# Optimization experiments

Hardware: AMD Instinct MI355X
Metric: run time of the kernel (lower is better)

## Reference

```python
import math
import jax, jax.numpy as jnp
import numpy as np

NHID = 1024
HEADS = 16
SEQ = 1024
BATCH = 8


def setup_inputs() -> dict:
    key = jax.random.key(0)
    ks = jax.random.split(key, 12)
    s = 0.02
    inp = {
        "query": jax.random.normal(ks[0], (SEQ, BATCH, NHID), jnp.float32),
        "key": jax.random.normal(ks[1], (SEQ, BATCH, NHID), jnp.float32),
        "value": jax.random.normal(ks[2], (SEQ, BATCH, NHID), jnp.float32),
        "qs_p": jax.random.normal(ks[3], (1, 1, NHID), jnp.float32) * s,
        "ks_p": jax.random.normal(ks[4], (1, 1, NHID), jnp.float32) * s,
        "vs_p": jax.random.normal(ks[5], (1, 1, NHID), jnp.float32) * s,
        "Wq": jax.random.normal(ks[6], (NHID, NHID), jnp.float32) * s,
        "bq": jax.random.normal(ks[7], (NHID,), jnp.float32) * s,
        "Wzf": jax.random.normal(ks[8], (2 * NHID, NHID), jnp.float32) * s,
        "bzf": jax.random.normal(ks[9], (2 * NHID,), jnp.float32) * s,
    }
    # additive causal mask, viewed as (1,1,S,S) and added to scores
    causal = jnp.triu(jnp.ones((SEQ, SEQ), jnp.float32), k=1) * (-1e9)
    inp["attn_mask"] = causal
    return inp


def reference(query, key, value, qs_p, ks_p, vs_p, Wq, bq, Wzf, bzf, attn_mask):
    nhid = NHID
    heads = HEADS
    dim = nhid // heads

    # sigmoid gates on Q/K/V scales
    qs = jax.nn.sigmoid(qs_p)              # (1,1,nhid)
    ks_g = jax.nn.sigmoid(ks_p)
    vs_in = jax.nn.sigmoid(vs_p)

    # QRNNLayer(window=1, output_gate=False) on single-step vs:
    # z = tanh(Wz vs + bz), f = sigmoid(Wf vs + bf), h = f * z (h0 = 0)
    zf = jnp.einsum('abn,mn->abm', vs_in, Wzf) + bzf   # (1,1,2*nhid)
    z = jnp.tanh(zf[..., :nhid])
    f = jax.nn.sigmoid(zf[..., nhid:])
    vs = f * z                                          # (1,1,nhid)

    # q projection (k,v have no Linear with defaults)
    q_lin = jnp.einsum('sbn,mn->sbm', query, Wq) + bq

    q = qs * q_lin       # (S,B,nhid)
    k = ks_g * key
    v = vs * value

    # seq-first -> batch-first, split heads
    def split_heads(t):
        t = t.transpose(1, 0, 2)                         # (B,S,nhid)
        B, S, _ = t.shape
        return t.reshape(B, S, heads, dim).transpose(0, 2, 1, 3)  # (B,H,S,d)

    qh, kh, vh = split_heads(q), split_heads(k), split_heads(v)

    scores = jnp.einsum('bhqd,bhkd->bhqk', qh, kh) / math.sqrt(dim)
    scores = scores + attn_mask[None, None]              # (B,H,S,S)
    weights = jax.nn.softmax(scores, axis=-1)
    mix = jnp.einsum('bhqk,bhkd->bhqd', weights, vh)     # (B,H,S,d)

    B = mix.shape[0]
    mix = mix.transpose(0, 2, 1, 3).reshape(B, -1, nhid)  # (B,S,nhid)
    mix = mix.transpose(1, 0, 2)                          # (S,B,nhid) seq-first
    return mix, weights
```

## Files before the change

kernel.cpp:

```cpp
#include <hip/hip_runtime.h>

typedef unsigned short u16;
typedef unsigned int   u32;
typedef float  f32x4  __attribute__((ext_vector_type(4)));
typedef short  bf16x8 __attribute__((ext_vector_type(8)));
typedef unsigned short u16x8 __attribute__((ext_vector_type(8)));
typedef unsigned short u16x4 __attribute__((ext_vector_type(4)));
typedef unsigned int   u32x2 __attribute__((ext_vector_type(2)));

#define DEV __device__ __forceinline__

constexpr int S  = 1024;
constexpr int BB = 8;
constexpr int NH = 1024;
constexpr int H  = 16;

DEV u16 f2bf(float f) {
  union { float f; unsigned u; } v{f};
  unsigned r = v.u + 0x7FFFu + ((v.u >> 16) & 1u);
  return (u16)(r >> 16);
}
DEV float sigm(float x) { return 1.0f / (1.0f + __expf(-x)); }

DEV void gload_lds16(const void* g, void* l) {
  __builtin_amdgcn_global_load_lds(
      (const __attribute__((address_space(1))) unsigned int*)g,
      (__attribute__((address_space(3))) unsigned int*)l, 16, 0, 0);
}

__global__ __launch_bounds__(256) void k_gates(
    const float* __restrict__ qs_p, const float* __restrict__ ks_p,
    const float* __restrict__ vs_p, const float* __restrict__ Wq,
    const float* __restrict__ bq,  const float* __restrict__ Wzf,
    const float* __restrict__ bzf,
    float* __restrict__ ksg, float* __restrict__ vsg,
    float* __restrict__ bq2, u16* __restrict__ wq_bf)
{
  int m = blockIdx.x * 4 + (threadIdx.x >> 6);
  int l = threadIdx.x & 63;
  const float* wz = Wzf + (size_t)m * NH;
  const float* wf = Wzf + (size_t)(m + NH) * NH;
  int base = l * 16;
  float za = 0.f, fa = 0.f;
#pragma unroll
  for (int i = 0; i < 16; i += 4) {
    float4 vp  = *(const float4*)(vs_p + base + i);
    float4 wzv = *(const float4*)(wz + base + i);
    float4 wfv = *(const float4*)(wf + base + i);
    float v0 = sigm(vp.x), v1 = sigm(vp.y), v2 = sigm(vp.z), v3 = sigm(vp.w);
    za += v0 * wzv.x + v1 * wzv.y + v2 * wzv.z + v3 * wzv.w;
    fa += v0 * wfv.x + v1 * wfv.y + v2 * wfv.z + v3 * wfv.w;
  }
#pragma unroll
  for (int off = 1; off < 64; off <<= 1) {
    za += __shfl_xor(za, off);
    fa += __shfl_xor(fa, off);
  }
  float z   = tanhf(za + bzf[m]);
  float f   = sigm(fa + bzf[m + NH]);
  float qsm = sigm(qs_p[m]);
  if (l == 0) {
    ksg[m] = sigm(ks_p[m]);
    vsg[m] = f * z;
    bq2[m] = qsm * bq[m];
  }
  const float* wqr = Wq + (size_t)m * NH;
  u16* dst = wq_bf + (size_t)m * NH + base;
#pragma unroll
  for (int i = 0; i < 16; i += 4) {
    float4 wv = *(const float4*)(wqr + base + i);
    u16x4 o;
    o[0] = f2bf(qsm * wv.x); o[1] = f2bf(qsm * wv.y);
    o[2] = f2bf(qsm * wv.z); o[3] = f2bf(qsm * wv.w);
    *(u16x4*)(dst + i) = o;
  }
}

__global__ __launch_bounds__(256) void k_prep(
    const float* __restrict__ query, const float* __restrict__ key,
    const float* __restrict__ value, const float* __restrict__ ksg,
    const float* __restrict__ vsg,
    u16* __restrict__ qx, u16* __restrict__ kout, u16* __restrict__ vout)
{
  __shared__ float tile[64][65];
  size_t idx = ((size_t)blockIdx.x * 256 + threadIdx.x) * 8;
  {
    float4 a = *(const float4*)(query + idx);
    float4 b = *(const float4*)(query + idx + 4);
    u16x8 o;
    o[0] = f2bf(a.x); o[1] = f2bf(a.y); o[2] = f2bf(a.z); o[3] = f2bf(a.w);
    o[4] = f2bf(b.x); o[5] = f2bf(b.y); o[6] = f2bf(b.z); o[7] = f2bf(b.w);
    *(u16x8*)(qx + idx) = o;
  }
  {
    int n0 = (int)(idx & 1023);
    int b  = (int)((idx >> 10) & 7);
    int s  = (int)(idx >> 13);
    float4 a  = *(const float4*)(key + idx);
    float4 c  = *(const float4*)(key + idx + 4);
    float4 g0 = *(const float4*)(ksg + n0);
    float4 g1 = *(const float4*)(ksg + n0 + 4);
    int h = n0 >> 6, d0 = n0 & 63;
    u16* dst = kout + (((size_t)(b * H + h) * S + s) * 64 + d0);
    u16x8 o;
    o[0] = f2bf(a.x * g0.x); o[1] = f2bf(a.y * g0.y);
    o[2] = f2bf(a.z * g0.z); o[3] = f2bf(a.w * g0.w);
    o[4] = f2bf(c.x * g1.x); o[5] = f2bf(c.y * g1.y);
    o[6] = f2bf(c.z * g1.z); o[7] = f2bf(c.w * g1.w);
    *(u16x8*)dst = o;
  }
  if (blockIdx.x < 2048) {
    int bh = blockIdx.x >> 4, kt = blockIdx.x & 15;
    int b = bh >> 4, h = bh & 15;
    int t = threadIdx.x;
    int sp = t >> 2, c0 = (t & 3) * 16;
    const float* src = value + ((size_t)(kt * 64 + sp) * (BB * NH) + b * NH + h * 64 + c0);
#pragma unroll
    for (int i = 0; i < 16; i += 4) {
      float4 v = *(const float4*)(src + i);
      float4 g = *(const float4*)(vsg + h * 64 + c0 + i);
      tile[sp][c0 + i + 0] = v.x * g.x;
      tile[sp][c0 + i + 1] = v.y * g.y;
      tile[sp][c0 + i + 2] = v.z * g.z;
      tile[sp][c0 + i + 3] = v.w * g.w;
    }
    __syncthreads();
    int d = t >> 2, s0 = (t & 3) * 16;
    u16* dst = vout + (((size_t)bh * 16 + kt) * 64 + d) * 64 + s0;
    u16x8 o0, o1;
#pragma unroll
    for (int i = 0; i < 8; ++i) o0[i] = f2bf(tile[s0 + i][d]);
#pragma unroll
    for (int i = 0; i < 8; ++i) o1[i] = f2bf(tile[s0 + 8 + i][d]);
    *(u16x8*)dst       = o0;
    *(u16x8*)(dst + 8) = o1;
  }
}

__global__ __launch_bounds__(256) void k_gemm_q(
    const u16* __restrict__ qx, const u16* __restrict__ wq,
    const float* __restrict__ bq2, u16* __restrict__ qws)
{
  __shared__ __align__(16) u16 As[128 * 64];
  __shared__ __align__(16) u16 Bs[128 * 64];
  int bid = blockIdx.x;
  int swz = (bid & 7) * 64 + (bid >> 3);
  int bx = swz & 7, by = swz >> 3;
  int tid = threadIdx.x, w = tid >> 6, l = tid & 63;
  int wr = w >> 1, wc = w & 1;
  f32x4 zero4 = {0.f, 0.f, 0.f, 0.f};
  f32x4 acc[4][4];
#pragma unroll
  for (int fi = 0; fi < 4; ++fi)
#pragma unroll
    for (int fj = 0; fj < 4; ++fj) acc[fi][fj] = zero4;

  for (int kt = 0; kt < 16; ++kt) {
    __syncthreads();
#pragma unroll
    for (int ii = 0; ii < 4; ++ii) {
      int i = w * 4 + ii;
      int row = i * 8 + (l >> 3);
      int blk = (l & 7) ^ (row & 7);
      gload_lds16(qx + ((size_t)(by * 128 + row) * 1024 + kt * 64 + blk * 8), &As[i * 512]);
      gload_lds16(wq + ((size_t)(bx * 128 + row) * 1024 + kt * 64 + blk * 8), &Bs[i * 512]);
    }
    __syncthreads();
#pragma unroll
    for (int kk = 0; kk < 2; ++kk) {
      bf16x8 av[4], bv[4];
#pragma unroll
      for (int f = 0; f < 4; ++f) {
        int ar = wr * 64 + f * 16 + (l & 15);
        av[f] = *(const bf16x8*)&As[ar * 64 + ((((kk << 2) + (l >> 4)) ^ (ar & 7)) << 3)];
        int br = wc * 64 + f * 16 + (l & 15);
        bv[f] = *(const bf16x8*)&Bs[br * 64 + ((((kk << 2) + (l >> 4)) ^ (br & 7)) << 3)];
      }
#pragma unroll
      for (int fi = 0; fi < 4; ++fi)
#pragma unroll
        for (int fj = 0; fj < 4; ++fj)
          acc[fi][fj] = __builtin_amdgcn_mfma_f32_16x16x32_bf16(av[fi], bv[fj], acc[fi][fj], 0, 0, 0);
    }
  }
#pragma unroll
  for (int fi = 0; fi < 4; ++fi) {
    int grb = by * 128 + wr * 64 + fi * 16 + ((l >> 4) << 2);
#pragma unroll
    for (int fj = 0; fj < 4; ++fj) {
      int mcol = bx * 128 + wc * 64 + fj * 16 + (l & 15);
      float badd = bq2[mcol];
      int h = mcol >> 6, d = mcol & 63;
#pragma unroll
      for (int r = 0; r < 4; ++r) {
        int gr = grb + r;
        int srow = gr >> 3, bb = gr & 7;
        qws[((size_t)(bb * H + h) * S + srow) * 64 + d] = f2bf(acc[fi][fj][r] + badd);
      }
    }
  }
}

__global__ __launch_bounds__(256) void k_attn(
    const u16* __restrict__ qws, const u16* __restrict__ kws,
    const u16* __restrict__ vtw, float* __restrict__ mix,
    float* __restrict__ wout)
{
  __shared__ __align__(16) u16 Ks[2][64 * 64];
  __shared__ __align__(16) u16 Vs[2][64 * 64];
  __shared__ __align__(16) u16 Ps[4][16 * 64];
  int bid = blockIdx.x;
  int swz = (bid & 7) * 256 + (bid >> 3);
  int qt = swz & 15, bh = swz >> 4;
  int tid = threadIdx.x, w = tid >> 6, l = tid & 63;
  int g = l >> 4, lq = l & 15;
  int q0 = qt * 64;
  int myq = q0 + 16 * w + lq;
  float* wbase = wout + (size_t)bh * S * S;

  auto stageK = [&](int kt, int buf) {
#pragma unroll
    for (int ii = 0; ii < 2; ++ii) {
      int i = w * 2 + ii;
      int row = i * 8 + (l >> 3);
      int blk = (l & 7) ^ (row & 7);
      gload_lds16(kws + ((size_t)bh * S + kt * 64 + row) * 64 + blk * 8, &Ks[buf][i * 512]);
    }
  };
  auto stageV = [&](int kt, int buf) {
#pragma unroll
    for (int ii = 0; ii < 2; ++ii) {
      int i = w * 2 + ii;
      int row = i * 8 + (l >> 3);
      int blk = (l & 7) ^ (row & 7);
      gload_lds16(vtw + (((size_t)bh * 16 + kt) * 64 + row) * 64 + blk * 8, &Vs[buf][i * 512]);
    }
  };

#pragma unroll
  for (int ii = 0; ii < 2; ++ii) {
    int i = w * 2 + ii;
    int row = i * 8 + (l >> 3);
    int blk = (l & 7) ^ (row & 7);
    gload_lds16(qws + ((size_t)bh * S + q0 + row) * 64 + blk * 8, &Ks[0][i * 512]);
  }
  asm volatile("s_waitcnt vmcnt(0)" ::: "memory");
  __builtin_amdgcn_sched_barrier(0);
  bf16x8 qa[2];
#pragma unroll
  for (int kk = 0; kk < 2; ++kk) {
    int qr = 16 * w + lq;
    qa[kk] = *(const bf16x8*)&Ks[0][qr * 64 + ((((kk << 2) + g) ^ (qr & 7)) << 3)];
  }
  asm volatile("s_waitcnt lgkmcnt(0)" ::: "memory");
  __builtin_amdgcn_sched_barrier(0);
  __builtin_amdgcn_s_barrier();

  stageK(0, 0);
  float lsum = 0.f;
  int cur = 0;
  for (int kt = 0; kt <= qt; ++kt) {
    asm volatile("s_waitcnt vmcnt(0)" ::: "memory");
    __builtin_amdgcn_sched_barrier(0);
    __builtin_amdgcn_s_barrier();
    __builtin_amdgcn_sched_barrier(0);
    if (kt < qt) stageK(kt + 1, cur ^ 1);
    __builtin_amdgcn_sched_barrier(0);
    f32x4 sacc[4];
    f32x4 zero4 = {0.f, 0.f, 0.f, 0.f};
#pragma unroll
    for (int fj = 0; fj < 4; ++fj) sacc[fj] = zero4;
#pragma unroll
    for (int kk = 0; kk < 2; ++kk)
#pragma unroll
      for (int fj = 0; fj < 4; ++fj) {
        int kr = fj * 16 + lq;
        bf16x8 kb = *(const bf16x8*)&Ks[cur][kr * 64 + ((((kk << 2) + g) ^ (kr & 7)) << 3)];
        sacc[fj] = __builtin_amdgcn_mfma_f32_16x16x32_bf16(kb, qa[kk], sacc[fj], 0, 0, 0);
      }
    if (kt < qt) {
#pragma unroll
      for (int fj = 0; fj < 4; ++fj)
#pragma unroll
        for (int r = 0; r < 4; ++r) lsum += __expf(sacc[fj][r] * 0.125f);
    } else {
#pragma unroll
      for (int fj = 0; fj < 4; ++fj)
#pragma unroll
        for (int r = 0; r < 4; ++r) {
          int ki = kt * 64 + fj * 16 + 4 * g + r;
          if (ki <= myq) lsum += __expf(sacc[fj][r] * 0.125f);
        }
    }
    cur ^= 1;
  }
  lsum += __shfl_xor(lsum, 16);
  lsum += __shfl_xor(lsum, 32);
  float invl = 1.0f / lsum;

  __builtin_amdgcn_s_barrier();

  stageK(0, 0);
  stageV(0, 0);
  cur = 0;
  f32x4 oacc[4];
  {
    f32x4 zero4 = {0.f, 0.f, 0.f, 0.f};
#pragma unroll
    for (int db = 0; db < 4; ++db) oacc[db] = zero4;
  }
  char* pb = (char*)&Ps[w][0];
  int pswz = (lq & 7) * 16;
  for (int kt = 0; kt <= qt; ++kt) {
    if (kt > 0) asm volatile("s_waitcnt vmcnt(4)" ::: "memory");
    else        asm volatile("s_waitcnt vmcnt(0)" ::: "memory");
    __builtin_amdgcn_sched_barrier(0);
    __builtin_amdgcn_s_barrier();
    __builtin_amdgcn_sched_barrier(0);
    if (kt < qt) { stageK(kt + 1, cur ^ 1); stageV(kt + 1, cur ^ 1); }
    __builtin_amdgcn_sched_barrier(0);
    f32x4 sacc[4];
    f32x4 zero4 = {0.f, 0.f, 0.f, 0.f};
#pragma unroll
    for (int fj = 0; fj < 4; ++fj) sacc[fj] = zero4;
#pragma unroll
    for (int kk = 0; kk < 2; ++kk)
#pragma unroll
      for (int fj = 0; fj < 4; ++fj) {
        int kr = fj * 16 + lq;
        bf16x8 kb = *(const bf16x8*)&Ks[cur][kr * 64 + ((((kk << 2) + g) ^ (kr & 7)) << 3)];
        sacc[fj] = __builtin_amdgcn_mfma_f32_16x16x32_bf16(kb, qa[kk], sacc[fj], 0, 0, 0);
      }
    float p0[4], p1[4], p2[4], p3[4];
    bool diag = (kt == qt);
#pragma unroll
    for (int fj = 0; fj < 4; ++fj) {
      float* pp = fj == 0 ? p0 : fj == 1 ? p1 : fj == 2 ? p2 : p3;
#pragma unroll
      for (int r = 0; r < 4; ++r) {
        float e = __expf(sacc[fj][r] * 0.125f) * invl;
        if (diag) {
          int ki = kt * 64 + fj * 16 + 4 * g + r;
          if (ki > myq) e = 0.f;
        }
        pp[r] = e;
      }
    }
#pragma unroll
    for (int fj = 0; fj < 4; ++fj) {
      float* pp = fj == 0 ? p0 : fj == 1 ? p1 : fj == 2 ? p2 : p3;
      u32 w0, w1;
      asm("v_cvt_pk_bf16_f32 %0, %1, %2" : "=v"(w0) : "v"(pp[0]), "v"(pp[1]));
      asm("v_cvt_pk_bf16_f32 %0, %1, %2" : "=v"(w1) : "v"(pp[2]), "v"(pp[3]));
      u32x2 wv = {w0, w1};
      *(u32x2*)(pb + lq * 128 + ((fj * 32 + g * 8) ^ pswz)) = wv;
    }
#pragma unroll
    for (int fj = 0; fj < 4; ++fj) {
      float* pp = fj == 0 ? p0 : fj == 1 ? p1 : fj == 2 ? p2 : p3;
      float4 f4 = {pp[0], pp[1], pp[2], pp[3]};
      *(float4*)(wbase + (size_t)myq * S + kt * 64 + fj * 16 + g * 4) = f4;
    }
    asm volatile("s_waitcnt lgkmcnt(0)" ::: "memory");
    __builtin_amdgcn_sched_barrier(0);
#pragma unroll
    for (int kk = 0; kk < 2; ++kk) {
      bf16x8 pa = *(const bf16x8*)(pb + lq * 128 + ((kk * 64 + g * 16) ^ pswz));
#pragma unroll
      for (int db = 0; db < 4; ++db) {
        int d = db * 16 + lq;
        bf16x8 vb = *(const bf16x8*)&Vs[cur][d * 64 + ((((kk << 2) + g) ^ (d & 7)) << 3)];
        oacc[db] = __builtin_amdgcn_mfma_f32_16x16x32_bf16(pa, vb, oacc[db], 0, 0, 0);
      }
    }
    cur ^= 1;
  }

  int b = bh >> 4, h = bh & 15;
#pragma unroll
  for (int db = 0; db < 4; ++db) {
#pragma unroll
    for (int r = 0; r < 4; ++r) {
      int qi = q0 + 16 * w + 4 * g + r;
      mix[(size_t)(qi * BB + b) * NH + h * 64 + db * 16 + lq] = oacc[db][r];
    }
  }

  {
    float4 z4 = {0.f, 0.f, 0.f, 0.f};
    for (int lr = 0; lr < 16; ++lr) {
      float* rowp = wbase + (size_t)(q0 + 16 * w + lr) * S;
      for (int c = (qt + 1) * 64 + l * 4; c < S; c += 256)
        *(float4*)(rowp + c) = z4;
    }
  }
}

extern "C" void kernel_launch(void* const* d_in, const int* in_sizes, int n_in,
                              void* d_out, int out_size, void* d_ws, size_t ws_size,
                              hipStream_t stream) {
  (void)in_sizes; (void)n_in; (void)out_size; (void)ws_size;
  const float* query = (const float*)d_in[0];
  const float* key   = (const float*)d_in[1];
  const float* value = (const float*)d_in[2];
  const float* qs_p  = (const float*)d_in[3];
  const float* ks_p  = (const float*)d_in[4];
  const float* vs_p  = (const float*)d_in[5];
  const float* Wq    = (const float*)d_in[6];
  const float* bq    = (const float*)d_in[7];
  const float* Wzf   = (const float*)d_in[8];
  const float* bzf   = (const float*)d_in[9];

  char* ws = (char*)d_ws;
  float* ksg  = (float*)(ws + 0x1000);
  float* vsg  = (float*)(ws + 0x2000);
  float* bq2  = (float*)(ws + 0x3000);
  u16* wq_bf  = (u16*)(ws + 0x4000);
  u16* qx_bf  = (u16*)(ws + 0x204000);
  u16* q_ws   = (u16*)(ws + 0x1204000);
  u16* k_ws   = (u16*)(ws + 0x2204000);
  u16* vt_ws  = (u16*)(ws + 0x3204000);

  float* mix  = (float*)d_out;
  float* wout = mix + (size_t)S * BB * NH;

  k_gates<<<256, 256, 0, stream>>>(qs_p, ks_p, vs_p, Wq, bq, Wzf, bzf,
                                   ksg, vsg, bq2, wq_bf);
  k_prep<<<4096, 256, 0, stream>>>(query, key, value, ksg, vsg,
                                   qx_bf, k_ws, vt_ws);
  k_gemm_q<<<512, 256, 0, stream>>>(qx_bf, wq_bf, bq2, q_ws);
  k_attn<<<2048, 256, 0, stream>>>(q_ws, k_ws, vt_ws, mix, wout);
}
```

Measured before the change: 226.9 us.

## Enlarge attention query tiles, pipeline K loads deeper, offload mask zeroing to GEMM

The attention kernel now processes 128 query rows per 512-thread block, with a 4-buffer K ring in the first pass and separate K and V double buffers in the second. The 1/sqrt(d)*log2(e) scale is folded into Q so raw v_exp_f32 can be used. Zero-filling of part of the upper-triangle weights is moved into the Q GEMM kernel to overlap it with compute. The change also adds nontemporal loads and stores and MFMA priority hints. The larger blocks halve the grid size and raise LDS and register pressure, and the hard-coded tile mapping for the offloaded zeroing is fragile.

```diff
diff --git a/kernel.cpp b/kernel.cpp
--- a/kernel.cpp
+++ b/kernel.cpp
@@ -21,11 +21,19 @@
   return (u16)(r >> 16);
 }
 DEV float sigm(float x) { return 1.0f / (1.0f + __expf(-x)); }
+DEV float exp2a(float x) { float r; asm("v_exp_f32 %0, %1" : "=v"(r) : "v"(x)); return r; }
 
 DEV void gload_lds16(const void* g, void* l) {
   __builtin_amdgcn_global_load_lds(
       (const __attribute__((address_space(1))) unsigned int*)g,
       (__attribute__((address_space(3))) unsigned int*)l, 16, 0, 0);
+}
+
+DEV f32x4 ntload4(const float* p) {
+  return __builtin_nontemporal_load((const f32x4*)p);
+}
+DEV void ntstore4(f32x4 v, float* p) {
+  __builtin_nontemporal_store(v, (f32x4*)p);
 }
 
 __global__ __launch_bounds__(256) void k_gates(
@@ -44,9 +52,9 @@
   float za = 0.f, fa = 0.f;
 #pragma unroll
   for (int i = 0; i < 16; i += 4) {
-    float4 vp  = *(const float4*)(vs_p + base + i);
-    float4 wzv = *(const float4*)(wz + base + i);
-    float4 wfv = *(const float4*)(wf + base + i);
+    f32x4 vp  = *(const f32x4*)(vs_p + base + i);
+    f32x4 wzv = *(const f32x4*)(wz + base + i);
+    f32x4 wfv = *(const f32x4*)(wf + base + i);
     float v0 = sigm(vp.x), v1 = sigm(vp.y), v2 = sigm(vp.z), v3 = sigm(vp.w);
     za += v0 * wzv.x + v1 * wzv.y + v2 * wzv.z + v3 * wzv.w;
     fa += v0 * wfv.x + v1 * wfv.y + v2 * wfv.z + v3 * wfv.w;
@@ -68,7 +76,7 @@
   u16* dst = wq_bf + (size_t)m * NH + base;
 #pragma unroll
   for (int i = 0; i < 16; i += 4) {
-    float4 wv = *(const float4*)(wqr + base + i);
+    f32x4 wv = *(const f32x4*)(wqr + base + i);
     u16x4 o;
     o[0] = f2bf(qsm * wv.x); o[1] = f2bf(qsm * wv.y);
     o[2] = f2bf(qsm * wv.z); o[3] = f2bf(qsm * wv.w);
@@ -85,8 +93,8 @@
   __shared__ float tile[64][65];
   size_t idx = ((size_t)blockIdx.x * 256 + threadIdx.x) * 8;
   {
-    float4 a = *(const float4*)(query + idx);
-    float4 b = *(const float4*)(query + idx + 4);
+    f32x4 a = ntload4(query + idx);
+    f32x4 b = ntload4(query + idx + 4);
     u16x8 o;
     o[0] = f2bf(a.x); o[1] = f2bf(a.y); o[2] = f2bf(a.z); o[3] = f2bf(a.w);
     o[4] = f2bf(b.x); o[5] = f2bf(b.y); o[6] = f2bf(b.z); o[7] = f2bf(b.w);
@@ -96,10 +104,10 @@
     int n0 = (int)(idx & 1023);
     int b  = (int)((idx >> 10) & 7);
     int s  = (int)(idx >> 13);
-    float4 a  = *(const float4*)(key + idx);
-    float4 c  = *(const float4*)(key + idx + 4);
-    float4 g0 = *(const float4*)(ksg + n0);
-    float4 g1 = *(const float4*)(ksg + n0 + 4);
+    f32x4 a  = ntload4(key + idx);
+    f32x4 c  = ntload4(key + idx + 4);
+    f32x4 g0 = *(const f32x4*)(ksg + n0);
+    f32x4 g1 = *(const f32x4*)(ksg + n0 + 4);
     int h = n0 >> 6, d0 = n0 & 63;
     u16* dst = kout + (((size_t)(b * H + h) * S + s) * 64 + d0);
     u16x8 o;
@@ -117,8 +125,8 @@
     const float* src = value + ((size_t)(kt * 64 + sp) * (BB * NH) + b * NH + h * 64 + c0);
 #pragma unroll
     for (int i = 0; i < 16; i += 4) {
-      float4 v = *(const float4*)(src + i);
-      float4 g = *(const float4*)(vsg + h * 64 + c0 + i);
+      f32x4 v = ntload4(src + i);
+      f32x4 g = *(const f32x4*)(vsg + h * 64 + c0 + i);
       tile[sp][c0 + i + 0] = v.x * g.x;
       tile[sp][c0 + i + 1] = v.y * g.y;
       tile[sp][c0 + i + 2] = v.z * g.z;
@@ -139,7 +147,8 @@
 
 __global__ __launch_bounds__(256) void k_gemm_q(
     const u16* __restrict__ qx, const u16* __restrict__ wq,
-    const float* __restrict__ bq2, u16* __restrict__ qws)
+    const float* __restrict__ bq2, u16* __restrict__ qws,
+    float* __restrict__ wout)
 {
   __shared__ __align__(16) u16 As[128 * 64];
   __shared__ __align__(16) u16 Bs[128 * 64];
@@ -165,6 +174,24 @@
       gload_lds16(qx + ((size_t)(by * 128 + row) * 1024 + kt * 64 + blk * 8), &As[i * 512]);
       gload_lds16(wq + ((size_t)(bx * 128 + row) * 1024 + kt * 64 + blk * 8), &Bs[i * 512]);
     }
+#pragma unroll
+    for (int c2 = 0; c2 < 4; ++c2) {
+      int c = kt * 4 + c2;
+      if (c < 56) {
+        int ti = c >> 3;
+        int tile_id = bid * 7 + ti;
+        if (tile_id < 3328) {
+          int fbh = tile_id / 26;
+          int r = tile_id - fbh * 26;
+          int t2 = (r < 14) ? 0 : 1;
+          int j = t2 ? (r - 10) : (r + 2);
+          int q = ((c & 7) << 8) + tid;
+          float* dst = wout + (size_t)fbh * S * S + (size_t)(t2 * 128 + (q >> 4)) * S
+                       + j * 64 + (q & 15) * 4;
+          ntstore4(zero4, dst);
+        }
+      }
+    }
     __syncthreads();
 #pragma unroll
     for (int kk = 0; kk < 2; ++kk) {
@@ -183,6 +210,7 @@
           acc[fi][fj] = __builtin_amdgcn_mfma_f32_16x16x32_bf16(av[fi], bv[fj], acc[fi][fj], 0, 0, 0);
     }
   }
+  const float SC = 0.18033688f;
 #pragma unroll
   for (int fi = 0; fi < 4; ++fi) {
     int grb = by * 128 + wr * 64 + fi * 16 + ((l >> 4) << 2);
@@ -195,54 +223,51 @@
       for (int r = 0; r < 4; ++r) {
         int gr = grb + r;
         int srow = gr >> 3, bb = gr & 7;
-        qws[((size_t)(bb * H + h) * S + srow) * 64 + d] = f2bf(acc[fi][fj][r] + badd);
-      }
-    }
-  }
-}
-
-__global__ __launch_bounds__(256) void k_attn(
+        qws[((size_t)(bb * H + h) * S + srow) * 64 + d] = f2bf((acc[fi][fj][r] + badd) * SC);
+      }
+    }
+  }
+}
+
+__global__ __launch_bounds__(512, 4) void k_attn(
     const u16* __restrict__ qws, const u16* __restrict__ kws,
     const u16* __restrict__ vtw, float* __restrict__ mix,
     float* __restrict__ wout)
 {
-  __shared__ __align__(16) u16 Ks[2][64 * 64];
-  __shared__ __align__(16) u16 Vs[2][64 * 64];
-  __shared__ __align__(16) u16 Ps[4][16 * 64];
+  __shared__ __align__(16) u16 KV[4][64 * 64];
+  __shared__ __align__(16) u16 Ps[8][16 * 64];
   int bid = blockIdx.x;
-  int swz = (bid & 7) * 256 + (bid >> 3);
-  int qt = swz & 15, bh = swz >> 4;
+  int swz = (bid & 7) * 128 + (bid >> 3);
+  int t = swz & 7, bh = swz >> 3;
   int tid = threadIdx.x, w = tid >> 6, l = tid & 63;
   int g = l >> 4, lq = l & 15;
-  int q0 = qt * 64;
+  int q0 = t * 128;
   int myq = q0 + 16 * w + lq;
+  int jmax = 2 * t + 1;
+  int jd = 2 * t + (w >> 2);
   float* wbase = wout + (size_t)bh * S * S;
-
-  auto stageK = [&](int kt, int buf) {
-#pragma unroll
-    for (int ii = 0; ii < 2; ++ii) {
-      int i = w * 2 + ii;
-      int row = i * 8 + (l >> 3);
-      int blk = (l & 7) ^ (row & 7);
-      gload_lds16(kws + ((size_t)bh * S + kt * 64 + row) * 64 + blk * 8, &Ks[buf][i * 512]);
-    }
+  u16* KVf = &KV[0][0];
+  int srow = l >> 3, sblk = l & 7;
+
+  auto stageK = [&](int j, int buf) {
+    int row = w * 8 + srow;
+    int blk = sblk ^ (row & 7);
+    gload_lds16(kws + ((size_t)bh * S + j * 64 + row) * 64 + blk * 8,
+                &KVf[buf * 4096 + w * 512]);
   };
-  auto stageV = [&](int kt, int buf) {
-#pragma unroll
-    for (int ii = 0; ii < 2; ++ii) {
-      int i = w * 2 + ii;
-      int row = i * 8 + (l >> 3);
-      int blk = (l & 7) ^ (row & 7);
-      gload_lds16(vtw + (((size_t)bh * 16 + kt) * 64 + row) * 64 + blk * 8, &Vs[buf][i * 512]);
-    }
+  auto stageV = [&](int j, int buf) {
+    int row = w * 8 + srow;
+    int blk = sblk ^ (row & 7);
+    gload_lds16(vtw + (((size_t)bh * 16 + j) * 64 + row) * 64 + blk * 8,
+                &KVf[buf * 4096 + w * 512]);
   };
 
 #pragma unroll
   for (int ii = 0; ii < 2; ++ii) {
     int i = w * 2 + ii;
-    int row = i * 8 + (l >> 3);
-    int blk = (l & 7) ^ (row & 7);
-    gload_lds16(qws + ((size_t)bh * S + q0 + row) * 64 + blk * 8, &Ks[0][i * 512]);
+    int row = i * 8 + srow;
+    int blk = sblk ^ (row & 7);
+    gload_lds16(qws + ((size_t)bh * S + q0 + row) * 64 + blk * 8, &KVf[i * 512]);
   }
   asm volatile("s_waitcnt vmcnt(0)" ::: "memory");
   __builtin_amdgcn_sched_barrier(0);
@@ -250,49 +275,56 @@
 #pragma unroll
   for (int kk = 0; kk < 2; ++kk) {
     int qr = 16 * w + lq;
-    qa[kk] = *(const bf16x8*)&Ks[0][qr * 64 + ((((kk << 2) + g) ^ (qr & 7)) << 3)];
+    qa[kk] = *(const bf16x8*)&KVf[qr * 64 + ((((kk << 2) + g) ^ (qr & 7)) << 3)];
   }
   asm volatile("s_waitcnt lgkmcnt(0)" ::: "memory");
   __builtin_amdgcn_sched_barrier(0);
   __builtin_amdgcn_s_barrier();
 
   stageK(0, 0);
+  if (jmax >= 1) stageK(1, 1);
+  if (jmax >= 2) stageK(2, 2);
   float lsum = 0.f;
-  int cur = 0;
-  for (int kt = 0; kt <= qt; ++kt) {
-    asm volatile("s_waitcnt vmcnt(0)" ::: "memory");
+  for (int j = 0; j <= jmax; ++j) {
+    if (j + 2 <= jmax)      asm volatile("s_waitcnt vmcnt(2)" ::: "memory");
+    else if (j + 1 <= jmax) asm volatile("s_waitcnt vmcnt(1)" ::: "memory");
+    else                    asm volatile("s_waitcnt vmcnt(0)" ::: "memory");
     __builtin_amdgcn_sched_barrier(0);
     __builtin_amdgcn_s_barrier();
     __builtin_amdgcn_sched_barrier(0);
-    if (kt < qt) stageK(kt + 1, cur ^ 1);
-    __builtin_amdgcn_sched_barrier(0);
-    f32x4 sacc[4];
-    f32x4 zero4 = {0.f, 0.f, 0.f, 0.f};
-#pragma unroll
-    for (int fj = 0; fj < 4; ++fj) sacc[fj] = zero4;
-#pragma unroll
-    for (int kk = 0; kk < 2; ++kk)
-#pragma unroll
-      for (int fj = 0; fj < 4; ++fj) {
-        int kr = fj * 16 + lq;
-        bf16x8 kb = *(const bf16x8*)&Ks[cur][kr * 64 + ((((kk << 2) + g) ^ (kr & 7)) << 3)];
-        sacc[fj] = __builtin_amdgcn_mfma_f32_16x16x32_bf16(kb, qa[kk], sacc[fj], 0, 0, 0);
-      }
-    if (kt < qt) {
-#pragma unroll
-      for (int fj = 0; fj < 4; ++fj)
-#pragma unroll
-        for (int r = 0; r < 4; ++r) lsum += __expf(sacc[fj][r] * 0.125f);
-    } else {
-#pragma unroll
-      for (int fj = 0; fj < 4; ++fj)
-#pragma unroll
-        for (int r = 0; r < 4; ++r) {
-          int ki = kt * 64 + fj * 16 + 4 * g + r;
-          if (ki <= myq) lsum += __expf(sacc[fj][r] * 0.125f);
+    if (j + 3 <= jmax) stageK(j + 3, (j + 3) & 3);
+    __builtin_amdgcn_sched_barrier(0);
+    if (j <= jd) {
+      int jb = (j & 3) * 4096;
+      f32x4 sacc[4];
+      f32x4 zero4 = {0.f, 0.f, 0.f, 0.f};
+#pragma unroll
+      for (int fj = 0; fj < 4; ++fj) sacc[fj] = zero4;
+      __builtin_amdgcn_s_setprio(1);
+#pragma unroll
+      for (int kk = 0; kk < 2; ++kk)
+#pragma unroll
+        for (int fj = 0; fj < 4; ++fj) {
+          int kr = fj * 16 + lq;
+          bf16x8 kb = *(const bf16x8*)&KVf[jb + kr * 64 + ((((kk << 2) + g) ^ (kr & 7)) << 3)];
+          sacc[fj] = __builtin_amdgcn_mfma_f32_16x16x32_bf16(kb, qa[kk], sacc[fj], 0, 0, 0);
         }
-    }
-    cur ^= 1;
+      __builtin_amdgcn_s_setprio(0);
+      if (j < jd) {
+#pragma unroll
+        for (int fj = 0; fj < 4; ++fj)
+#pragma unroll
+          for (int r = 0; r < 4; ++r) lsum += exp2a(sacc[fj][r]);
+      } else {
+#pragma unroll
+        for (int fj = 0; fj < 4; ++fj)
+#pragma unroll
+          for (int r = 0; r < 4; ++r) {
+            int ki = j * 64 + fj * 16 + 4 * g + r;
+            if (ki <= myq) lsum += exp2a(sacc[fj][r]);
+          }
+      }
+    }
   }
   lsum += __shfl_xor(lsum, 16);
   lsum += __shfl_xor(lsum, 32);
@@ -301,8 +333,8 @@
   __builtin_amdgcn_s_barrier();
 
   stageK(0, 0);
-  stageV(0, 0);
-  cur = 0;
+  stageV(0, 2);
+  int cur = 0;
   f32x4 oacc[4];
   {
     f32x4 zero4 = {0.f, 0.f, 0.f, 0.f};
@@ -311,67 +343,79 @@
   }
   char* pb = (char*)&Ps[w][0];
   int pswz = (lq & 7) * 16;
-  for (int kt = 0; kt <= qt; ++kt) {
-    if (kt > 0) asm volatile("s_waitcnt vmcnt(4)" ::: "memory");
-    else        asm volatile("s_waitcnt vmcnt(0)" ::: "memory");
+  for (int j = 0; j <= jmax; ++j) {
+    if (j == 0) asm volatile("s_waitcnt vmcnt(0)" ::: "memory");
+    else        asm volatile("s_waitcnt vmcnt(4)" ::: "memory");
     __builtin_amdgcn_sched_barrier(0);
     __builtin_amdgcn_s_barrier();
     __builtin_amdgcn_sched_barrier(0);
-    if (kt < qt) { stageK(kt + 1, cur ^ 1); stageV(kt + 1, cur ^ 1); }
-    __builtin_amdgcn_sched_barrier(0);
-    f32x4 sacc[4];
-    f32x4 zero4 = {0.f, 0.f, 0.f, 0.f};
-#pragma unroll
-    for (int fj = 0; fj < 4; ++fj) sacc[fj] = zero4;
-#pragma unroll
-    for (int kk = 0; kk < 2; ++kk)
+    if (j < jmax) { stageK(j + 1, cur ^ 1); stageV(j + 1, 2 + (cur ^ 1)); }
+    __builtin_amdgcn_sched_barrier(0);
+    if (j > jd) {
+      f32x4 z4 = {0.f, 0.f, 0.f, 0.f};
+#pragma unroll
+      for (int fj = 0; fj < 4; ++fj)
+        ntstore4(z4, wbase + (size_t)myq * S + j * 64 + fj * 16 + g * 4);
+    } else {
+      int kbase = cur * 4096;
+      f32x4 sacc[4];
+      f32x4 zero4 = {0.f, 0.f, 0.f, 0.f};
+#pragma unroll
+      for (int fj = 0; fj < 4; ++fj) sacc[fj] = zero4;
+      __builtin_amdgcn_s_setprio(1);
+#pragma unroll
+      for (int kk = 0; kk < 2; ++kk)
+#pragma unroll
+        for (int fj = 0; fj < 4; ++fj) {
+          int kr = fj * 16 + lq;
+          bf16x8 kb = *(const bf16x8*)&KVf[kbase + kr * 64 + ((((kk << 2) + g) ^ (kr & 7)) << 3)];
+          sacc[fj] = __builtin_amdgcn_mfma_f32_16x16x32_bf16(kb, qa[kk], sacc[fj], 0, 0, 0);
+        }
+      __builtin_amdgcn_s_setprio(0);
+      bool diag = (j == jd);
+      float p0[4], p1[4], p2[4], p3[4];
 #pragma unroll
       for (int fj = 0; fj < 4; ++fj) {
-        int kr = fj * 16 + lq;
-        bf16x8 kb = *(const bf16x8*)&Ks[cur][kr * 64 + ((((kk << 2) + g) ^ (kr & 7)) << 3)];
-        sacc[fj] = __builtin_amdgcn_mfma_f32_16x16x32_bf16(kb, qa[kk], sacc[fj], 0, 0, 0);
-      }
-    float p0[4], p1[4], p2[4], p3[4];
-    bool diag = (kt == qt);
-#pragma unroll
-    for (int fj = 0; fj < 4; ++fj) {
-      float* pp = fj == 0 ? p0 : fj == 1 ? p1 : fj == 2 ? p2 : p3;
-#pragma unroll
-      for (int r = 0; r < 4; ++r) {
-        float e = __expf(sacc[fj][r] * 0.125f) * invl;
-        if (diag) {
-          int ki = kt * 64 + fj * 16 + 4 * g + r;
-          if (ki > myq) e = 0.f;
+        float* pp = fj == 0 ? p0 : fj == 1 ? p1 : fj == 2 ? p2 : p3;
+#pragma unroll
+        for (int r = 0; r < 4; ++r) {
+          float e = exp2a(sacc[fj][r]) * invl;
+          if (diag) {
+            int ki = j * 64 + fj * 16 + 4 * g + r;
+            if (ki > myq) e = 0.f;
+          }
+          pp[r] = e;
         }
-        pp[r] = e;
-      }
-    }
-#pragma unroll
-    for (int fj = 0; fj < 4; ++fj) {
-      float* pp = fj == 0 ? p0 : fj == 1 ? p1 : fj == 2 ? p2 : p3;
-      u32 w0, w1;
-      asm("v_cvt_pk_bf16_f32 %0, %1, %2" : "=v"(w0) : "v"(pp[0]), "v"(pp[1]));
-      asm("v_cvt_pk_bf16_f32 %0, %1, %2" : "=v"(w1) : "v"(pp[2]), "v"(pp[3]));
-      u32x2 wv = {w0, w1};
-      *(u32x2*)(pb + lq * 128 + ((fj * 32 + g * 8) ^ pswz)) = wv;
-    }
-#pragma unroll
-    for (int fj = 0; fj < 4; ++fj) {
-      float* pp = fj == 0 ? p0 : fj == 1 ? p1 : fj == 2 ? p2 : p3;
-      float4 f4 = {pp[0], pp[1], pp[2], pp[3]};
-      *(float4*)(wbase + (size_t)myq * S + kt * 64 + fj * 16 + g * 4) = f4;
-    }
-    asm volatile("s_waitcnt lgkmcnt(0)" ::: "memory");
-    __builtin_amdgcn_sched_barrier(0);
-#pragma unroll
-    for (int kk = 0; kk < 2; ++kk) {
-      bf16x8 pa = *(const bf16x8*)(pb + lq * 128 + ((kk * 64 + g * 16) ^ pswz));
-#pragma unroll
-      for (int db = 0; db < 4; ++db) {
-        int d = db * 16 + lq;
-        bf16x8 vb = *(const bf16x8*)&Vs[cur][d * 64 + ((((kk << 2) + g) ^ (d & 7)) << 3)];
-        oacc[db] = __builtin_amdgcn_mfma_f32_16x16x32_bf16(pa, vb, oacc[db], 0, 0, 0);
-      }
+      }
+#pragma unroll
+      for (int fj = 0; fj < 4; ++fj) {
+        float* pp = fj == 0 ? p0 : fj == 1 ? p1 : fj == 2 ? p2 : p3;
+        u32 w0, w1;
+        asm("v_cvt_pk_bf16_f32 %0, %1, %2" : "=v"(w0) : "v"(pp[0]), "v"(pp[1]));
+        asm("v_cvt_pk_bf16_f32 %0, %1, %2" : "=v"(w1) : "v"(pp[2]), "v"(pp[3]));
+        u32x2 wv = {w0, w1};
+        *(u32x2*)(pb + lq * 128 + ((fj * 32 + g * 8) ^ pswz)) = wv;
+      }
+#pragma unroll
+      for (int fj = 0; fj < 4; ++fj) {
+        float* pp = fj == 0 ? p0 : fj == 1 ? p1 : fj == 2 ? p2 : p3;
+        f32x4 f4 = {pp[0], pp[1], pp[2], pp[3]};
+        ntstore4(f4, wbase + (size_t)myq * S + j * 64 + fj * 16 + g * 4);
+      }
+      asm volatile("s_waitcnt lgkmcnt(0)" ::: "memory");
+      __builtin_amdgcn_sched_barrier(0);
+      __builtin_amdgcn_s_setprio(1);
+#pragma unroll
+      for (int kk = 0; kk < 2; ++kk) {
+        bf16x8 pa = *(const bf16x8*)(pb + lq * 128 + ((kk * 64 + g * 16) ^ pswz));
+#pragma unroll
+        for (int db = 0; db < 4; ++db) {
+          int d = db * 16 + lq;
+          bf16x8 vb = *(const bf16x8*)&KVf[(2 + cur) * 4096 + d * 64 + ((((kk << 2) + g) ^ (d & 7)) << 3)];
+          oacc[db] = __builtin_amdgcn_mfma_f32_16x16x32_bf16(pa, vb, oacc[db], 0, 0, 0);
+        }
+      }
+      __builtin_amdgcn_s_setprio(0);
     }
     cur ^= 1;
   }
@@ -382,16 +426,18 @@
 #pragma unroll
     for (int r = 0; r < 4; ++r) {
       int qi = q0 + 16 * w + 4 * g + r;
-      mix[(size_t)(qi * BB + b) * NH + h * 64 + db * 16 + lq] = oacc[db][r];
-    }
-  }
-
-  {
-    float4 z4 = {0.f, 0.f, 0.f, 0.f};
+      __builtin_nontemporal_store(oacc[db][r],
+          mix + (size_t)(qi * BB + b) * NH + h * 64 + db * 16 + lq);
+    }
+  }
+
+  if (t >= 2) {
+    f32x4 z4 = {0.f, 0.f, 0.f, 0.f};
+    int cstart = (jmax + 1) * 64;
     for (int lr = 0; lr < 16; ++lr) {
       float* rowp = wbase + (size_t)(q0 + 16 * w + lr) * S;
-      for (int c = (qt + 1) * 64 + l * 4; c < S; c += 256)
-        *(float4*)(rowp + c) = z4;
+      for (int c = cstart + l * 4; c < S; c += 256)
+        ntstore4(z4, rowp + c);
     }
   }
 }
@@ -428,6 +474,6 @@
                                    ksg, vsg, bq2, wq_bf);
   k_prep<<<4096, 256, 0, stream>>>(query, key, value, ksg, vsg,
                                    qx_bf, k_ws, vt_ws);
-  k_gemm_q<<<512, 256, 0, stream>>>(qx_bf, wq_bf, bq2, q_ws);
-  k_attn<<<2048, 256, 0, stream>>>(q_ws, k_ws, vt_ws, mix, wout);
-}
+  k_gemm_q<<<512, 256, 0, stream>>>(qx_bf, wq_bf, bq2, q_ws, wout);
+  k_attn<<<1024, 512, 0, stream>>>(q_ws, k_ws, vt_ws, mix, wout);
+}
```

Result: no change. 227.3 us (+0.2%).
